# Kernel tuning notes

Measured on AMD Instinct MI355X. Metric: run time of the kernel, lower is better.

Reference implementation:

```python
import jax, jax.numpy as jnp
import numpy as np

# Hard-concrete gate constants (module defaults)
TEMP = 2.0 / 3.0          # gate_temperature
STRETCH_EPS = 0.1         # gate_stretch_epsilon -> stretch to [-0.1, 1.1]
PRE_CLIP = 2.0            # gate_pre_activation_clip

N_NODES = 100000
N_CLUSTERS = 32
N_RELATIONS = 8
N_EDGES = 500000


def _hard_concrete_gate_eval(log_alpha):
    # eval-mode sample: deterministic, pre = log_alpha / temperature
    pre = jnp.clip(log_alpha / TEMP, -PRE_CLIP, PRE_CLIP)
    lo, hi = -STRETCH_EPS, 1.0 + STRETCH_EPS
    z = jax.nn.sigmoid(pre) * (hi - lo) + lo
    return jnp.clip(z, 0.0, 1.0)


def setup_inputs() -> dict:
    key = jax.random.key(0)
    k0, k1, k2, k3, k4, k5 = jax.random.split(key, 6)
    assignments = jax.random.normal(k0, (N_NODES, N_CLUSTERS), dtype=jnp.float32)
    edge_index = jax.random.randint(k1, (2, N_EDGES), 0, N_NODES, dtype=jnp.int64)
    edge_type = jax.random.randint(k2, (N_EDGES,), 0, N_RELATIONS, dtype=jnp.int64)
    inter_cluster_logits = jax.random.normal(k3, (N_RELATIONS, N_CLUSTERS, N_CLUSTERS), dtype=jnp.float32)
    gate_log_alpha = jax.random.normal(k4, (N_RELATIONS, N_CLUSTERS, N_CLUSTERS), dtype=jnp.float32)
    absent_bias = jax.random.normal(k5, (N_RELATIONS,), dtype=jnp.float32) * 0.1
    return {
        "assignments": assignments,
        "edge_index": edge_index,
        "edge_type": edge_type,
        "inter_cluster_logits": inter_cluster_logits,
        "gate_log_alpha": gate_log_alpha,
        "absent_bias": absent_bias,
    }


def reference(assignments, edge_index, edge_type, inter_cluster_logits, gate_log_alpha, absent_bias):
    # weights = sigmoid(logits) * hard_concrete_gate(log_alpha)   [R, K, K]
    weights = jax.nn.sigmoid(inter_cluster_logits) * _hard_concrete_gate_eval(gate_log_alpha)
    src = assignments[edge_index[0]]   # [E, K]
    dst = assignments[edge_index[1]]   # [E, K]
    # weighted_dst[e] = weights[edge_type[e]] @ dst[e]
    # compute all-relation products then gather (avoids materializing [E,K,K])
    wd_all = jnp.einsum('ej,rij->eri', dst, weights)            # [E, R, K]
    weighted_dst = jnp.take_along_axis(wd_all, edge_type[:, None, None], axis=1)[:, 0, :]  # [E, K]
    logits = jnp.sum(src * weighted_dst, axis=-1) + absent_bias[edge_type]  # [E]
    return logits
```

## Files before the change

kernel.cpp:

```cpp
#include <hip/hip_runtime.h>
#include <hip/hip_bf16.h>
#include <cstdint>

#define KDIM 32
#define RMAX 8
#define NBLK 256

typedef _Float16 half2v __attribute__((ext_vector_type(2)));
typedef _Float16 half4v __attribute__((ext_vector_type(4)));
typedef float    f32x4  __attribute__((ext_vector_type(4)));

#if __has_builtin(__builtin_amdgcn_mfma_f32_16x16x16f16)
#define USE_MFMA 1
#else
#define USE_MFMA 0
#endif

__device__ __forceinline__ float sigmoidf_(float x) {
    return 1.0f / (1.0f + expf(-x));
}

__device__ __forceinline__ float gate_weight_(float logit, float log_alpha) {
    float pre = log_alpha * 1.5f;
    pre = fminf(fmaxf(pre, -2.0f), 2.0f);
    float z = sigmoidf_(pre) * 1.2f - 0.1f;
    z = fminf(fmaxf(z, 0.0f), 1.0f);
    return sigmoidf_(logit) * z;
}

__global__ __launch_bounds__(256) void prep_kernel(
    const int* __restrict__ et, int E, int chunk,
    int* __restrict__ bh , int R,
    const float* __restrict__ logits, const float* __restrict__ la,
    _Float16* __restrict__ Wh, int n,
    const float* __restrict__ A, _Float16* __restrict__ Ah, int nA) {
    int g = blockIdx.x * blockDim.x + threadIdx.x;
    if (g < n) Wh[g] = (_Float16)gate_weight_(logits[g], la[g]);

    int nthreads = gridDim.x * blockDim.x;
    int n4 = nA >> 2;
    for (int i4 = g; i4 < n4; i4 += nthreads) {
        float4 v = ((const float4*)A)[i4];
        half2v h0; h0[0] = (_Float16)v.x; h0[1] = (_Float16)v.y;
        half2v h1; h1[0] = (_Float16)v.z; h1[1] = (_Float16)v.w;
        ((half2v*)Ah)[i4 * 2 + 0] = h0;
        ((half2v*)Ah)[i4 * 2 + 1] = h1;
    }

    __shared__ int h[RMAX];
    if ((int)threadIdx.x < RMAX) h[threadIdx.x] = 0;
    __syncthreads();
    int b = blockIdx.x;
    int start = b * chunk;
    int end = start + chunk;
    if (end > E) end = E;
    for (int i = start + threadIdx.x; i < end; i += blockDim.x) {
        atomicAdd(&h[et[i]], 1);
    }
    __syncthreads();
    if ((int)threadIdx.x < RMAX) bh[b * RMAX + threadIdx.x] = h[threadIdx.x];
}

__global__ __launch_bounds__(512) void scan2_kernel(
    int* __restrict__ bh, int* __restrict__ off,
    int4* __restrict__ edata, int R) {
    __shared__ int tr[RMAX][NBLK];
    __shared__ int cnt_s[RMAX];
    __shared__ int off_s[RMAX + 1];
    int t = threadIdx.x;

    for (int i = t; i < NBLK * RMAX; i += 512) {
        int b = i / RMAX, r = i % RMAX;
        tr[r][b] = bh[i];
    }
    __syncthreads();

    int w = t >> 6;
    int lane = t & 63;
    if (w < R) {
        int b0 = lane * 4;
        int v0 = tr[w][b0 + 0];
        int v1 = tr[w][b0 + 1];
        int v2 = tr[w][b0 + 2];
        int v3 = tr[w][b0 + 3];
        int s0 = v0, s1 = s0 + v1, s2 = s1 + v2, s3 = s2 + v3;
        int lanesum = s3;
        int sc = lanesum;
#pragma unroll
        for (int d = 1; d < 64; d <<= 1) {
            int up = __shfl_up(sc, d, 64);
            if (lane >= d) sc += up;
        }
        int excl = sc - lanesum;
        tr[w][b0 + 0] = excl;
        tr[w][b0 + 1] = excl + s0;
        tr[w][b0 + 2] = excl + s1;
        tr[w][b0 + 3] = excl + s2;
        if (lane == 63) cnt_s[w] = sc;
    }
    __syncthreads();

    if (t == 0) {
        int o = 0;
        off_s[0] = 0;
        for (int r = 0; r < R; r++) {
            o += (cnt_s[r] + 63) & ~63;
            off_s[r + 1] = o;
        }
        for (int r = 0; r <= R; r++) off[r] = off_s[r];
    }
    __syncthreads();

    for (int i = t; i < NBLK * RMAX; i += 512) {
        int b = i / RMAX, r = i % RMAX;
        bh[i] = tr[r][b] + ((r < R) ? off_s[r] : 0);
    }
    for (int r = 0; r < R; r++) {
        int padStart = off_s[r] + cnt_s[r];
        int padEnd = off_s[r + 1];
        for (int i = padStart + t; i < padEnd; i += 512) {
            edata[i] = make_int4(0, 0, -1, 0);
        }
    }
}

__global__ __launch_bounds__(256) void scatter3_kernel(
    const int* __restrict__ et, const int* __restrict__ ei, int E, int chunk,
    const int* __restrict__ bh, int4* __restrict__ edata, int R) {
    __shared__ int cur[RMAX];
    int b = blockIdx.x;
    if ((int)threadIdx.x < RMAX) cur[threadIdx.x] = bh[b * RMAX + threadIdx.x];
    __syncthreads();
    int start = b * chunk;
    int end = start + chunk;
    if (end > E) end = E;
    for (int i = start + threadIdx.x; i < end; i += blockDim.x) {
        int r = et[i];
        int sn = ei[i];
        int dn = ei[E + i];
        int pos = atomicAdd(&cur[r], 1);
        edata[pos] = make_int4(sn, dn, i, 0);
    }
}

#if USE_MFMA
__global__ __launch_bounds__(256) void gather4_kernel(
    const _Float16* __restrict__ Ah, const _Float16* __restrict__ Wh,
    const float* __restrict__ bias, const int4* __restrict__ edata,
    const int* __restrict__ off, float* __restrict__ out, int capA, int R) {
    int g = blockIdx.x * blockDim.x + threadIdx.x;
    int lane = threadIdx.x & 63;
    int lm = lane & 15;
    int lg = lane >> 4;
    int kq = lg * 4;

    int r = 0;
    for (int rr = 1; rr < R; rr++) r += (g >= off[rr]) ? 1 : 0;
    r = __builtin_amdgcn_readfirstlane(r);
    float br = bias[r];

    const _Float16* Wr = Wh + (size_t)r * (KDIM * KDIM);
    half4v aw1 = *(const half4v*)(Wr + lm * KDIM + kq);
    half4v aw2 = *(const half4v*)(Wr + lm * KDIM + 16 + kq);
    half4v aw3 = *(const half4v*)(Wr + (16 + lm) * KDIM + kq);
    half4v aw4 = *(const half4v*)(Wr + (16 + lm) * KDIM + 16 + kq);

    int wbase = (blockIdx.x * blockDim.x + (threadIdx.x & ~63));
    f32x4 zeroF = {0.0f, 0.0f, 0.0f, 0.0f};
    bool diag_lane = (lg == (lm >> 2));

#pragma unroll
    for (int s = 0; s < 4; s++) {
        int4 rec = edata[wbase + s * 16 + lm];
        bool valid = (rec.z >= 0);
        int sn = valid ? rec.x : 0;
        int dn = valid ? rec.y : 0;

        const _Float16* Sp = Ah + (size_t)sn * KDIM;
        const _Float16* Dp = Ah + (size_t)dn * KDIM;
        half4v as1 = *(const half4v*)(Sp + kq);
        half4v as2 = *(const half4v*)(Sp + 16 + kq);
        half4v bd1 = *(const half4v*)(Dp + kq);
        half4v bd2 = *(const half4v*)(Dp + 16 + kq);

        f32x4 z1 = __builtin_amdgcn_mfma_f32_16x16x16f16(aw1, bd1, zeroF, 0, 0, 0);
        z1 = __builtin_amdgcn_mfma_f32_16x16x16f16(aw2, bd2, z1, 0, 0, 0);
        f32x4 z2 = __builtin_amdgcn_mfma_f32_16x16x16f16(aw3, bd1, zeroF, 0, 0, 0);
        z2 = __builtin_amdgcn_mfma_f32_16x16x16f16(aw4, bd2, z2, 0, 0, 0);

        half4v zb1, zb2;
        half2v t0 = __builtin_bit_cast(half2v, __builtin_amdgcn_cvt_pkrtz(z1[0], z1[1]));
        half2v t1 = __builtin_bit_cast(half2v, __builtin_amdgcn_cvt_pkrtz(z1[2], z1[3]));
        half2v t2 = __builtin_bit_cast(half2v, __builtin_amdgcn_cvt_pkrtz(z2[0], z2[1]));
        half2v t3 = __builtin_bit_cast(half2v, __builtin_amdgcn_cvt_pkrtz(z2[2], z2[3]));
        zb1[0] = t0[0]; zb1[1] = t0[1]; zb1[2] = t1[0]; zb1[3] = t1[1];
        zb2[0] = t2[0]; zb2[1] = t2[1]; zb2[2] = t3[0]; zb2[3] = t3[1];

        f32x4 c = __builtin_amdgcn_mfma_f32_16x16x16f16(as1, zb1, zeroF, 0, 0, 0);
        c = __builtin_amdgcn_mfma_f32_16x16x16f16(as2, zb2, c, 0, 0, 0);

        if (valid && diag_lane) out[rec.z] = c[lm & 3] + br;
    }
}
#else
__global__ __launch_bounds__(256) void gather4_kernel(
    const _Float16* __restrict__ Ah, const _Float16* __restrict__ Wh,
    const float* __restrict__ bias, const int4* __restrict__ edata,
    const int* __restrict__ off, float* __restrict__ out, int capA, int R) {
    int g = blockIdx.x * blockDim.x + threadIdx.x;
    if (g >= capA) return;

    int r = 0;
    for (int rr = 1; rr < R; rr++) r += (g >= off[rr]) ? 1 : 0;
    r = __builtin_amdgcn_readfirstlane(r);

    int4 rec = edata[g];
    bool valid = (rec.z >= 0);
    int sn = valid ? rec.x : 0;
    int dn = valid ? rec.y : 0;

    const uint4* As = (const uint4*)(Ah + (size_t)sn * KDIM);
    const uint4* Ad = (const uint4*)(Ah + (size_t)dn * KDIM);
    unsigned int sp[16], dp[16];
#pragma unroll
    for (int q = 0; q < 4; q++) {
        uint4 s4 = As[q];
        uint4 d4 = Ad[q];
        sp[4 * q + 0] = s4.x; sp[4 * q + 1] = s4.y;
        sp[4 * q + 2] = s4.z; sp[4 * q + 3] = s4.w;
        dp[4 * q + 0] = d4.x; dp[4 * q + 1] = d4.y;
        dp[4 * q + 2] = d4.z; dp[4 * q + 3] = d4.w;
    }

    const unsigned int* __restrict__ Wr =
        (const unsigned int*)(Wh + (size_t)r * (KDIM * KDIM));
    float total = 0.0f;
#pragma unroll
    for (int i = 0; i < KDIM; i++) {
        float acc = 0.0f;
#pragma unroll
        for (int j2 = 0; j2 < KDIM / 2; j2++) {
            half2v w = __builtin_bit_cast(half2v, Wr[i * 16 + j2]);
            half2v d = __builtin_bit_cast(half2v, dp[j2]);
#if __has_builtin(__builtin_amdgcn_fdot2)
            acc = __builtin_amdgcn_fdot2(w, d, acc, false);
#else
            acc = fmaf((float)w[0], (float)d[0], acc);
            acc = fmaf((float)w[1], (float)d[1], acc);
#endif
        }
        half2v s2 = __builtin_bit_cast(half2v, sp[i >> 1]);
        float sv = (float)s2[i & 1];
        total = fmaf(sv, acc, total);
    }

    if (valid) out[rec.z] = total + bias[r];
}
#endif

__global__ __launch_bounds__(256) void gather_unsorted_kernel(
    const float* __restrict__ A, const int* __restrict__ ei,
    const int* __restrict__ et,
    const float* __restrict__ logits, const float* __restrict__ la,
    const float* __restrict__ bias, float* __restrict__ out, int E, int R) {
    __shared__ float Wl[RMAX * 1032];
    int total_w = R * KDIM * KDIM;
    for (int t = threadIdx.x; t < total_w; t += blockDim.x) {
        int r = t / (KDIM * KDIM);
        int ij = t % (KDIM * KDIM);
        Wl[r * 1032 + ij] = gate_weight_(logits[t], la[t]);
    }
    __syncthreads();

    for (int e = blockIdx.x * blockDim.x + threadIdx.x; e < E;
         e += gridDim.x * blockDim.x) {
        int r = et[e];
        int sn = ei[e];
        int dn = ei[E + e];
        const float4* As = (const float4*)(A + (size_t)sn * KDIM);
        const float4* Ad = (const float4*)(A + (size_t)dn * KDIM);
        float sv[KDIM], dv[KDIM];
#pragma unroll
        for (int q = 0; q < KDIM / 4; q++) {
            float4 s4 = As[q];
            float4 d4 = Ad[q];
            sv[4 * q + 0] = s4.x; sv[4 * q + 1] = s4.y;
            sv[4 * q + 2] = s4.z; sv[4 * q + 3] = s4.w;
            dv[4 * q + 0] = d4.x; dv[4 * q + 1] = d4.y;
            dv[4 * q + 2] = d4.z; dv[4 * q + 3] = d4.w;
        }
        float totalv = 0.0f;
#pragma unroll
        for (int i = 0; i < KDIM; i++) {
            const float* Wrow = &Wl[r * 1032 + i * KDIM];
            float acc = 0.0f;
#pragma unroll
            for (int j = 0; j < KDIM / 4; j++) {
                float4 w4 = ((const float4*)Wrow)[j];
                acc = fmaf(w4.x, dv[4 * j + 0], acc);
                acc = fmaf(w4.y, dv[4 * j + 1], acc);
                acc = fmaf(w4.z, dv[4 * j + 2], acc);
                acc = fmaf(w4.w, dv[4 * j + 3], acc);
            }
            totalv = fmaf(sv[i], acc, totalv);
        }
        out[e] = totalv + bias[r];
    }
}

extern "C" void kernel_launch(void* const* d_in, const int* in_sizes, int n_in,
                              void* d_out, int out_size, void* d_ws, size_t ws_size,
                              hipStream_t stream) {
    const float* A      = (const float*)d_in[0];
    const int*   ei     = (const int*)d_in[1];
    const int*   et     = (const int*)d_in[2];
    const float* logits = (const float*)d_in[3];
    const float* la     = (const float*)d_in[4];
    const float* bias   = (const float*)d_in[5];
    float* out = (float*)d_out;

    int E = in_sizes[2];
    int R = in_sizes[5];
    int n = in_sizes[3];
    int nA = in_sizes[0];

    int capA = (E + 64 * RMAX + 255) & ~255;
    size_t ahb = ((size_t)nA * 2 + 15) & ~(size_t)15;
    size_t edata_off = 16384 + 64 + (size_t)NBLK * RMAX * 4 + ahb;
    size_t need = edata_off + (size_t)capA * 16;

    if (R <= RMAX && ws_size >= need) {
        char* ws = (char*)d_ws;
        _Float16* Wh = (_Float16*)(ws);
        int* off     = (int*)(ws + 16384);
        int* bh      = (int*)(ws + 16384 + 64);
        _Float16* Ah = (_Float16*)(ws + 16384 + 64 + NBLK * RMAX * 4);
        int4* edata  = (int4*)(ws + edata_off);

        int chunk = (E + NBLK - 1) / NBLK;

        prep_kernel<<<NBLK, 256, 0, stream>>>(
            et, E, chunk, bh, R, logits, la, Wh, n, A, Ah, nA);
        scan2_kernel<<<1, 512, 0, stream>>>(bh, off, edata, R);
        scatter3_kernel<<<NBLK, 256, 0, stream>>>(et, ei, E, chunk, bh, edata, R);
        gather4_kernel<<<capA / 256, 256, 0, stream>>>(
            Ah, Wh, bias, edata, off, out, capA, R);
    } else {
        int gblocks = (E + 255) / 256;
        if (gblocks > 2048) gblocks = 2048;
        gather_unsorted_kernel<<<gblocks, 256, 0, stream>>>(
            A, ei, et, logits, la, bias, out, E, R);
    }
}
```

Before: 106.7 us.

## Fuse histogram, scan, scatter and MFMA gather into one per-block LDS-sorted kernel

Replaces the four-kernel pipeline (global histogram, single-block scan, global scatter into a padded edge array, MFMA gather) with a prep kernel plus one fused kernel. Each block counts relation types for its own chunk of about 512 edges, buckets them in shared memory padded to groups of 16, and runs the MFMA bilinear computation directly from LDS. This removes the global edata round trip, the serial scan launch and two launches. In exchange, padding is per block rather than global, so there are more partially filled 16-edge groups, and W fragments are reloaded for every group.

```diff
diff --git a/kernel.cpp b/kernel.cpp
--- a/kernel.cpp
+++ b/kernel.cpp
@@ -4,7 +4,8 @@
 
 #define KDIM 32
 #define RMAX 8
-#define NBLK 256
+#define CAPL 1280
+#define GMAX 128
 
 typedef _Float16 half2v __attribute__((ext_vector_type(2)));
 typedef _Float16 half4v __attribute__((ext_vector_type(4)));
@@ -28,9 +29,7 @@
     return sigmoidf_(logit) * z;
 }
 
-__global__ __launch_bounds__(256) void prep_kernel(
-    const int* __restrict__ et, int E, int chunk,
-    int* __restrict__ bh , int R,
+__global__ __launch_bounds__(256) void prep3_kernel(
     const float* __restrict__ logits, const float* __restrict__ la,
     _Float16* __restrict__ Wh, int n,
     const float* __restrict__ A, _Float16* __restrict__ Ah, int nA) {
@@ -46,135 +45,96 @@
         ((half2v*)Ah)[i4 * 2 + 0] = h0;
         ((half2v*)Ah)[i4 * 2 + 1] = h1;
     }
-
-    __shared__ int h[RMAX];
-    if ((int)threadIdx.x < RMAX) h[threadIdx.x] = 0;
-    __syncthreads();
+}
+
+#if USE_MFMA
+__global__ __launch_bounds__(256) void fused_kernel(
+    const _Float16* __restrict__ Ah, const _Float16* __restrict__ Wh,
+    const float* __restrict__ bias, const int* __restrict__ ei,
+    const int* __restrict__ et, float* __restrict__ out, int E, int chunk) {
+    __shared__ int sn_l[CAPL], dn_l[CAPL], e_l[CAPL];
+    __shared__ int cnt[RMAX], cur[RMAX], pb[RMAX + 1];
+    __shared__ int rg[GMAX];
+    __shared__ int ng_s;
+
+    int t = threadIdx.x;
     int b = blockIdx.x;
     int start = b * chunk;
     int end = start + chunk;
     if (end > E) end = E;
-    for (int i = start + threadIdx.x; i < end; i += blockDim.x) {
-        atomicAdd(&h[et[i]], 1);
-    }
-    __syncthreads();
-    if ((int)threadIdx.x < RMAX) bh[b * RMAX + threadIdx.x] = h[threadIdx.x];
-}
-
-__global__ __launch_bounds__(512) void scan2_kernel(
-    int* __restrict__ bh, int* __restrict__ off,
-    int4* __restrict__ edata, int R) {
-    __shared__ int tr[RMAX][NBLK];
-    __shared__ int cnt_s[RMAX];
-    __shared__ int off_s[RMAX + 1];
-    int t = threadIdx.x;
-
-    for (int i = t; i < NBLK * RMAX; i += 512) {
-        int b = i / RMAX, r = i % RMAX;
-        tr[r][b] = bh[i];
-    }
-    __syncthreads();
-
-    int w = t >> 6;
-    int lane = t & 63;
-    if (w < R) {
-        int b0 = lane * 4;
-        int v0 = tr[w][b0 + 0];
-        int v1 = tr[w][b0 + 1];
-        int v2 = tr[w][b0 + 2];
-        int v3 = tr[w][b0 + 3];
-        int s0 = v0, s1 = s0 + v1, s2 = s1 + v2, s3 = s2 + v3;
-        int lanesum = s3;
-        int sc = lanesum;
-#pragma unroll
-        for (int d = 1; d < 64; d <<= 1) {
-            int up = __shfl_up(sc, d, 64);
-            if (lane >= d) sc += up;
-        }
-        int excl = sc - lanesum;
-        tr[w][b0 + 0] = excl;
-        tr[w][b0 + 1] = excl + s0;
-        tr[w][b0 + 2] = excl + s1;
-        tr[w][b0 + 3] = excl + s2;
-        if (lane == 63) cnt_s[w] = sc;
+
+    if (t < RMAX) cnt[t] = 0;
+    __syncthreads();
+
+    for (int i = start + t; i < end; i += 256) {
+        atomicAdd(&cnt[et[i]], 1);
     }
     __syncthreads();
 
     if (t == 0) {
         int o = 0;
-        off_s[0] = 0;
-        for (int r = 0; r < R; r++) {
-            o += (cnt_s[r] + 63) & ~63;
-            off_s[r + 1] = o;
-        }
-        for (int r = 0; r <= R; r++) off[r] = off_s[r];
-    }
-    __syncthreads();
-
-    for (int i = t; i < NBLK * RMAX; i += 512) {
-        int b = i / RMAX, r = i % RMAX;
-        bh[i] = tr[r][b] + ((r < R) ? off_s[r] : 0);
-    }
-    for (int r = 0; r < R; r++) {
-        int padStart = off_s[r] + cnt_s[r];
-        int padEnd = off_s[r + 1];
-        for (int i = padStart + t; i < padEnd; i += 512) {
-            edata[i] = make_int4(0, 0, -1, 0);
-        }
-    }
-}
-
-__global__ __launch_bounds__(256) void scatter3_kernel(
-    const int* __restrict__ et, const int* __restrict__ ei, int E, int chunk,
-    const int* __restrict__ bh, int4* __restrict__ edata, int R) {
-    __shared__ int cur[RMAX];
-    int b = blockIdx.x;
-    if ((int)threadIdx.x < RMAX) cur[threadIdx.x] = bh[b * RMAX + threadIdx.x];
-    __syncthreads();
-    int start = b * chunk;
-    int end = start + chunk;
-    if (end > E) end = E;
-    for (int i = start + threadIdx.x; i < end; i += blockDim.x) {
+        pb[0] = 0;
+#pragma unroll
+        for (int r = 0; r < RMAX; r++) {
+            cur[r] = o;
+            o += (cnt[r] + 15) & ~15;
+            pb[r + 1] = o;
+        }
+        ng_s = o >> 4;
+    }
+    __syncthreads();
+
+    int ng = ng_s;
+    for (int g = t; g < ng; g += 256) {
+        int s16 = g << 4;
+        int r = 0;
+#pragma unroll
+        for (int rr = 1; rr < RMAX; rr++) r += (s16 >= pb[rr]) ? 1 : 0;
+        rg[g] = r;
+    }
+#pragma unroll
+    for (int r = 0; r < RMAX; r++) {
+        int ps = pb[r] + cnt[r];
+        int pe = pb[r + 1];
+        for (int i = ps + t; i < pe; i += 256) {
+            e_l[i] = -1; sn_l[i] = 0; dn_l[i] = 0;
+        }
+    }
+    for (int i = start + t; i < end; i += 256) {
         int r = et[i];
         int sn = ei[i];
         int dn = ei[E + i];
         int pos = atomicAdd(&cur[r], 1);
-        edata[pos] = make_int4(sn, dn, i, 0);
-    }
-}
-
-#if USE_MFMA
-__global__ __launch_bounds__(256) void gather4_kernel(
-    const _Float16* __restrict__ Ah, const _Float16* __restrict__ Wh,
-    const float* __restrict__ bias, const int4* __restrict__ edata,
-    const int* __restrict__ off, float* __restrict__ out, int capA, int R) {
-    int g = blockIdx.x * blockDim.x + threadIdx.x;
-    int lane = threadIdx.x & 63;
+        sn_l[pos] = sn; dn_l[pos] = dn; e_l[pos] = i;
+    }
+    __syncthreads();
+
+    int wid = t >> 6;
+    int lane = t & 63;
     int lm = lane & 15;
     int lg = lane >> 4;
     int kq = lg * 4;
-
-    int r = 0;
-    for (int rr = 1; rr < R; rr++) r += (g >= off[rr]) ? 1 : 0;
-    r = __builtin_amdgcn_readfirstlane(r);
-    float br = bias[r];
-
-    const _Float16* Wr = Wh + (size_t)r * (KDIM * KDIM);
-    half4v aw1 = *(const half4v*)(Wr + lm * KDIM + kq);
-    half4v aw2 = *(const half4v*)(Wr + lm * KDIM + 16 + kq);
-    half4v aw3 = *(const half4v*)(Wr + (16 + lm) * KDIM + kq);
-    half4v aw4 = *(const half4v*)(Wr + (16 + lm) * KDIM + 16 + kq);
-
-    int wbase = (blockIdx.x * blockDim.x + (threadIdx.x & ~63));
     f32x4 zeroF = {0.0f, 0.0f, 0.0f, 0.0f};
     bool diag_lane = (lg == (lm >> 2));
 
-#pragma unroll
-    for (int s = 0; s < 4; s++) {
-        int4 rec = edata[wbase + s * 16 + lm];
-        bool valid = (rec.z >= 0);
-        int sn = valid ? rec.x : 0;
-        int dn = valid ? rec.y : 0;
+    for (int g = wid; g < ng; g += 4) {
+        int r = rg[g];
+        r = __builtin_amdgcn_readfirstlane(r);
+        float br = bias[r];
+
+        const _Float16* Wr = Wh + (size_t)r * (KDIM * KDIM);
+        half4v aw1 = *(const half4v*)(Wr + lm * KDIM + kq);
+        half4v aw2 = *(const half4v*)(Wr + lm * KDIM + 16 + kq);
+        half4v aw3 = *(const half4v*)(Wr + (16 + lm) * KDIM + kq);
+        half4v aw4 = *(const half4v*)(Wr + (16 + lm) * KDIM + 16 + kq);
+
+        int slot = (g << 4) + lm;
+        int ev  = e_l[slot];
+        int snv = sn_l[slot];
+        int dnv = dn_l[slot];
+        bool valid = (ev >= 0);
+        int sn = valid ? snv : 0;
+        int dn = valid ? dnv : 0;
 
         const _Float16* Sp = Ah + (size_t)sn * KDIM;
         const _Float16* Dp = Ah + (size_t)dn * KDIM;
@@ -199,62 +159,8 @@
         f32x4 c = __builtin_amdgcn_mfma_f32_16x16x16f16(as1, zb1, zeroF, 0, 0, 0);
         c = __builtin_amdgcn_mfma_f32_16x16x16f16(as2, zb2, c, 0, 0, 0);
 
-        if (valid && diag_lane) out[rec.z] = c[lm & 3] + br;
-    }
-}
-#else
-__global__ __launch_bounds__(256) void gather4_kernel(
-    const _Float16* __restrict__ Ah, const _Float16* __restrict__ Wh,
-    const float* __restrict__ bias, const int4* __restrict__ edata,
-    const int* __restrict__ off, float* __restrict__ out, int capA, int R) {
-    int g = blockIdx.x * blockDim.x + threadIdx.x;
-    if (g >= capA) return;
-
-    int r = 0;
-    for (int rr = 1; rr < R; rr++) r += (g >= off[rr]) ? 1 : 0;
-    r = __builtin_amdgcn_readfirstlane(r);
-
-    int4 rec = edata[g];
-    bool valid = (rec.z >= 0);
-    int sn = valid ? rec.x : 0;
-    int dn = valid ? rec.y : 0;
-
-    const uint4* As = (const uint4*)(Ah + (size_t)sn * KDIM);
-    const uint4* Ad = (const uint4*)(Ah + (size_t)dn * KDIM);
-    unsigned int sp[16], dp[16];
-#pragma unroll
-    for (int q = 0; q < 4; q++) {
-        uint4 s4 = As[q];
-        uint4 d4 = Ad[q];
-        sp[4 * q + 0] = s4.x; sp[4 * q + 1] = s4.y;
-        sp[4 * q + 2] = s4.z; sp[4 * q + 3] = s4.w;
-        dp[4 * q + 0] = d4.x; dp[4 * q + 1] = d4.y;
-        dp[4 * q + 2] = d4.z; dp[4 * q + 3] = d4.w;
-    }
-
-    const unsigned int* __restrict__ Wr =
-        (const unsigned int*)(Wh + (size_t)r * (KDIM * KDIM));
-    float total = 0.0f;
-#pragma unroll
-    for (int i = 0; i < KDIM; i++) {
-        float acc = 0.0f;
-#pragma unroll
-        for (int j2 = 0; j2 < KDIM / 2; j2++) {
-            half2v w = __builtin_bit_cast(half2v, Wr[i * 16 + j2]);
-            half2v d = __builtin_bit_cast(half2v, dp[j2]);
-#if __has_builtin(__builtin_amdgcn_fdot2)
-            acc = __builtin_amdgcn_fdot2(w, d, acc, false);
-#else
-            acc = fmaf((float)w[0], (float)d[0], acc);
-            acc = fmaf((float)w[1], (float)d[1], acc);
-#endif
-        }
-        half2v s2 = __builtin_bit_cast(half2v, sp[i >> 1]);
-        float sv = (float)s2[i & 1];
-        total = fmaf(sv, acc, total);
-    }
-
-    if (valid) out[rec.z] = total + bias[r];
+        if (valid && diag_lane) out[ev] = c[lm & 3] + br;
+    }
 }
 #endif
 
@@ -324,27 +230,29 @@
     int n = in_sizes[3];
     int nA = in_sizes[0];
 
-    int capA = (E + 64 * RMAX + 255) & ~255;
-    size_t ahb = ((size_t)nA * 2 + 15) & ~(size_t)15;
-    size_t edata_off = 16384 + 64 + (size_t)NBLK * RMAX * 4 + ahb;
-    size_t need = edata_off + (size_t)capA * 16;
-
-    if (R <= RMAX && ws_size >= need) {
+    size_t need = 16384 + (size_t)nA * 2;
+
+    int nblk = (E + 511) / 512;
+    if (nblk > 2048) nblk = 2048;
+    if (nblk < 1) nblk = 1;
+    int chunk = (E + nblk - 1) / nblk;
+
+#if USE_MFMA
+    bool fast = (R <= RMAX) && ((nA & 3) == 0) && (ws_size >= need) &&
+                (chunk <= CAPL - 128);
+#else
+    bool fast = false;
+#endif
+
+    if (fast) {
+#if USE_MFMA
         char* ws = (char*)d_ws;
         _Float16* Wh = (_Float16*)(ws);
-        int* off     = (int*)(ws + 16384);
-        int* bh      = (int*)(ws + 16384 + 64);
-        _Float16* Ah = (_Float16*)(ws + 16384 + 64 + NBLK * RMAX * 4);
-        int4* edata  = (int4*)(ws + edata_off);
-
-        int chunk = (E + NBLK - 1) / NBLK;
-
-        prep_kernel<<<NBLK, 256, 0, stream>>>(
-            et, E, chunk, bh, R, logits, la, Wh, n, A, Ah, nA);
-        scan2_kernel<<<1, 512, 0, stream>>>(bh, off, edata, R);
-        scatter3_kernel<<<NBLK, 256, 0, stream>>>(et, ei, E, chunk, bh, edata, R);
-        gather4_kernel<<<capA / 256, 256, 0, stream>>>(
-            Ah, Wh, bias, edata, off, out, capA, R);
+        _Float16* Ah = (_Float16*)(ws + 16384);
+
+        prep3_kernel<<<512, 256, 0, stream>>>(logits, la, Wh, n, A, Ah, nA);
+        fused_kernel<<<nblk, 256, 0, stream>>>(Ah, Wh, bias, ei, et, out, E, chunk);
+#endif
     } else {
         int gblocks = (E + 255) / 256;
         if (gblocks > 2048) gblocks = 2048;
```

New measurement: 131.5 us. +23.2%, slower.
